# Performance work log

Measured on AMD Instinct MI355X. Metric: run time of the kernel, lower is better.

The kernel has to match this reference:

```python
import jax, jax.numpy as jnp
import numpy as np

N_NODES = 100000
N_EDGES = 3200000
N_FEAT = 512
HIDDEN = 16
N_CLASSES = 40


def gcn_conv(x, src, dst, W, b, num_nodes):
    # GCNConv with self-loops and symmetric normalization (default PyG settings).
    loop = jnp.arange(num_nodes)
    s = jnp.concatenate([src, loop])
    d = jnp.concatenate([dst, loop])
    deg = jax.ops.segment_sum(jnp.ones_like(s, dtype=x.dtype), d, num_segments=num_nodes)
    dinv = jnp.where(deg > 0, jax.lax.rsqrt(deg), 0.0)
    norm = dinv[s] * dinv[d]  # [E+N]
    h = x @ W  # [N, out]
    msg = h[s] * norm[:, None]  # gather + scale
    out = jax.ops.segment_sum(msg, d, num_segments=num_nodes)  # scatter-add
    return out + b


def setup_inputs() -> dict:
    key = jax.random.key(0)
    k1, k2, k3, k4 = jax.random.split(key, 4)
    x = jax.random.normal(k1, (N_NODES, N_FEAT), dtype=jnp.float32)
    edge_index = jax.random.randint(k2, (2, N_EDGES), 0, N_NODES, dtype=jnp.int64)
    W1 = jax.random.normal(k3, (N_FEAT, HIDDEN), dtype=jnp.float32) * 0.05
    b1 = jnp.zeros((HIDDEN,), dtype=jnp.float32)
    W2 = jax.random.normal(k4, (HIDDEN, N_CLASSES), dtype=jnp.float32) * 0.05
    b2 = jnp.zeros((N_CLASSES,), dtype=jnp.float32)
    return {"x": x, "edge_index": edge_index, "W1": W1, "b1": b1, "W2": W2, "b2": b2}


def reference(x, edge_index, W1, b1, W2, b2):
    num_nodes = x.shape[0]
    src, dst = edge_index[0], edge_index[1]
    h = gcn_conv(x, src, dst, W1, b1, num_nodes)
    h = jax.nn.relu(h)
    # dropout is identity in eval mode (training=False)
    out = gcn_conv(h, src, dst, W2, b2, num_nodes)
    return jax.nn.log_softmax(out, axis=1)
```

## Files before the change

kernel.cpp:

```cpp
#include <hip/hip_runtime.h>

#define N_NODES 100000
#define N_EDGES 3200000
#define N_FEAT 512
#define HIDDEN 16
#define N_CLASSES 40

#define SCAN_BLOCKS 98


__global__ void k_zero_int(int* p, int n) {
    int i = blockIdx.x * 256 + threadIdx.x;
    if (i < n) p[i] = 0;
}

__global__ void k_count(const int* __restrict__ dst, int* __restrict__ cnt,
                        int* __restrict__ ord) {
    int e = blockIdx.x * 256 + threadIdx.x;
    if (e < N_EDGES) ord[e] = atomicAdd(cnt + dst[e], 1);
}

__global__ void k_dinv(const int* __restrict__ cnt, float* __restrict__ dinv) {
    int i = blockIdx.x * 256 + threadIdx.x;
    if (i < N_NODES) dinv[i] = rsqrtf((float)(cnt[i] + 1));
}


__global__ __launch_bounds__(1024) void k_scan_a(const int* __restrict__ cnt,
                                                 int* __restrict__ bsum) {
    int tid = threadIdx.x;
    int i = blockIdx.x * 1024 + tid;
    int v = (i < N_NODES) ? cnt[i] : 0;
    #pragma unroll
    for (int off = 32; off >= 1; off >>= 1) v += __shfl_xor(v, off, 64);
    __shared__ int ws[16];
    if ((tid & 63) == 0) ws[tid >> 6] = v;
    __syncthreads();
    if (tid == 0) {
        int s = 0;
        #pragma unroll
        for (int w = 0; w < 16; w++) s += ws[w];
        bsum[blockIdx.x] = s;
    }
}

__global__ __launch_bounds__(128) void k_scan_b(const int* __restrict__ bsum,
                                                int* __restrict__ boff) {
    int tid = threadIdx.x;
    int lane = tid & 63, wv = tid >> 6;
    int v = (tid < SCAN_BLOCKS) ? bsum[tid] : 0;
    int sc = v;
    #pragma unroll
    for (int off = 1; off < 64; off <<= 1) {
        int t = __shfl_up(sc, off, 64);
        if (lane >= off) sc += t;
    }
    __shared__ int wsum[2];
    if (lane == 63) wsum[wv] = sc;
    __syncthreads();
    int pre = (wv == 1) ? wsum[0] : 0;
    if (tid < SCAN_BLOCKS) boff[tid] = pre + sc - v;
}

__global__ __launch_bounds__(1024) void k_scan_c(const int* __restrict__ cnt,
                                                 const int* __restrict__ boff,
                                                 int* __restrict__ row_start) {
    int tid = threadIdx.x;
    int i = blockIdx.x * 1024 + tid;
    int lane = tid & 63, wv = tid >> 6;
    int v = (i < N_NODES) ? cnt[i] : 0;
    int sc = v;
    #pragma unroll
    for (int off = 1; off < 64; off <<= 1) {
        int t = __shfl_up(sc, off, 64);
        if (lane >= off) sc += t;
    }
    __shared__ int wsum[16];
    if (lane == 63) wsum[wv] = sc;
    __syncthreads();
    int pre = 0;
    #pragma unroll
    for (int w = 0; w < 16; w++) pre += (w < wv) ? wsum[w] : 0;
    int excl = boff[blockIdx.x] + pre + sc - v;
    if (i < N_NODES) row_start[i] = excl;
    if (i == N_NODES) row_start[N_NODES] = N_EDGES;
}

__global__ void k_build(const int* __restrict__ src, const int* __restrict__ dst,
                        const int* __restrict__ ord, const int* __restrict__ row_start,
                        const float* __restrict__ dinv, int2* __restrict__ edge_data) {
    int e = blockIdx.x * 256 + threadIdx.x;
    if (e >= N_EDGES) return;
    int s = src[e], d = dst[e];
    int slot = row_start[d] + ord[e];
    float nrm = dinv[s] * dinv[d];
    edge_data[slot] = make_int2(s, __float_as_int(nrm));
}


#define KC 32
#define LDSW 36

__global__ __launch_bounds__(256) void k_gemm1(const float* __restrict__ x,
                                               const float* __restrict__ W1,
                                               float* __restrict__ h1) {
    __shared__ float xs[256 * LDSW];
    int tid = threadIdx.x;
    int row = blockIdx.x * 256 + tid;

    float acc[HIDDEN];
    #pragma unroll
    for (int j = 0; j < HIDDEN; j++) acc[j] = 0.f;

    int s_sub = tid >> 3;
    int s_k4  = tid & 7;

    for (int kc = 0; kc < N_FEAT; kc += KC) {
        __syncthreads();
        #pragma unroll
        for (int l = 0; l < 8; l++) {
            int srow = s_sub + l * 32;
            int grow = blockIdx.x * 256 + srow;
            int gr = grow < N_NODES ? grow : N_NODES - 1;
            float4 v = *reinterpret_cast<const float4*>(
                x + (size_t)gr * N_FEAT + kc + s_k4 * 4);
            *reinterpret_cast<float4*>(&xs[srow * LDSW + s_k4 * 4]) = v;
        }
        __syncthreads();

        const float* Wc = W1 + kc * HIDDEN;
        #pragma unroll
        for (int k4 = 0; k4 < 8; k4++) {
            float4 xv = *reinterpret_cast<const float4*>(&xs[tid * LDSW + k4 * 4]);
            const float* w0 = Wc + (k4 * 4 + 0) * HIDDEN;
            const float* w1 = Wc + (k4 * 4 + 1) * HIDDEN;
            const float* w2 = Wc + (k4 * 4 + 2) * HIDDEN;
            const float* w3 = Wc + (k4 * 4 + 3) * HIDDEN;
            #pragma unroll
            for (int j = 0; j < HIDDEN; j++) {
                acc[j] += xv.x * w0[j];
                acc[j] += xv.y * w1[j];
                acc[j] += xv.z * w2[j];
                acc[j] += xv.w * w3[j];
            }
        }
    }

    if (row < N_NODES) {
        float4* op = reinterpret_cast<float4*>(h1 + (size_t)row * HIDDEN);
        #pragma unroll
        for (int q = 0; q < 4; q++)
            op[q] = make_float4(acc[q*4+0], acc[q*4+1], acc[q*4+2], acc[q*4+3]);
    }
}


template <bool RELU>
__global__ __launch_bounds__(256) void k_agg16(const int2* __restrict__ edge_data,
                                               const int* __restrict__ row_start,
                                               const float* __restrict__ dinv,
                                               const float* __restrict__ h,
                                               const float* __restrict__ bias,
                                               float* __restrict__ out) {
    int g = threadIdx.x >> 4, j = threadIdx.x & 15;
    int node = blockIdx.x * 16 + g;
    if (node >= N_NODES) return;
    int beg = row_start[node], end = row_start[node + 1];
    float ds = dinv[node];
    float acc = h[(size_t)node * HIDDEN + j] * (ds * ds);
    int i = beg;
    for (; i + 3 < end; i += 4) {
        int2 e0 = edge_data[i + 0];
        int2 e1 = edge_data[i + 1];
        int2 e2 = edge_data[i + 2];
        int2 e3 = edge_data[i + 3];
        float v0 = h[(size_t)e0.x * HIDDEN + j];
        float v1 = h[(size_t)e1.x * HIDDEN + j];
        float v2 = h[(size_t)e2.x * HIDDEN + j];
        float v3 = h[(size_t)e3.x * HIDDEN + j];
        acc += v0 * __int_as_float(e0.y);
        acc += v1 * __int_as_float(e1.y);
        acc += v2 * __int_as_float(e2.y);
        acc += v3 * __int_as_float(e3.y);
    }
    for (; i < end; ++i) {
        int2 ed = edge_data[i];
        acc += h[(size_t)ed.x * HIDDEN + j] * __int_as_float(ed.y);
    }
    if (RELU) acc = fmaxf(acc + bias[j], 0.f);
    out[(size_t)node * HIDDEN + j] = acc;
}


__global__ __launch_bounds__(256) void k_out(const float* __restrict__ agg2,
                                             const float* __restrict__ W2,
                                             const float* __restrict__ b2,
                                             float* __restrict__ out) {
    int r = blockIdx.x * 256 + threadIdx.x;
    if (r >= N_NODES) return;
    float a[HIDDEN];
    const float4* ap = reinterpret_cast<const float4*>(agg2 + (size_t)r * HIDDEN);
    #pragma unroll
    for (int q = 0; q < 4; q++) {
        float4 v = ap[q];
        a[q * 4 + 0] = v.x; a[q * 4 + 1] = v.y;
        a[q * 4 + 2] = v.z; a[q * 4 + 3] = v.w;
    }
    float acc[N_CLASSES];
    #pragma unroll
    for (int jj = 0; jj < N_CLASSES; jj++) acc[jj] = b2[jj];
    #pragma unroll
    for (int kk = 0; kk < HIDDEN; kk++) {
        float av = a[kk];
        #pragma unroll
        for (int jj = 0; jj < N_CLASSES; jj++)
            acc[jj] += av * W2[kk * N_CLASSES + jj];
    }
    float m = -1e30f;
    #pragma unroll
    for (int jj = 0; jj < N_CLASSES; jj++) m = fmaxf(m, acc[jj]);
    float sum = 0.f;
    #pragma unroll
    for (int jj = 0; jj < N_CLASSES; jj++) sum += __expf(acc[jj] - m);
    float l = m + __logf(sum);
    float4* op = reinterpret_cast<float4*>(out + (size_t)r * N_CLASSES);
    #pragma unroll
    for (int q = 0; q < N_CLASSES / 4; q++) {
        op[q] = make_float4(acc[q*4+0] - l, acc[q*4+1] - l,
                            acc[q*4+2] - l, acc[q*4+3] - l);
    }
}


extern "C" void kernel_launch(void* const* d_in, const int* in_sizes, int n_in,
                              void* d_out, int out_size, void* d_ws, size_t ws_size,
                              hipStream_t stream) {
    const float* x  = (const float*)d_in[0];
    const int*   ei = (const int*)d_in[1];
    const float* W1 = (const float*)d_in[2];
    const float* b1 = (const float*)d_in[3];
    const float* W2 = (const float*)d_in[4];
    const float* b2 = (const float*)d_in[5];
    const int* src = ei;
    const int* dst = ei + N_EDGES;
    float* out = (float*)d_out;

    char* ws = (char*)d_ws;
    size_t off = 0;
    auto alloc = [&](size_t bytes) {
        size_t o = off; off = (off + bytes + 255) & ~(size_t)255; return o;
    };
    float* dinv      = (float*)(ws + alloc(sizeof(float) * N_NODES));
    int*   cnt       = (int*)  (ws + alloc(sizeof(int) * N_NODES));
    int*   row_start = (int*)  (ws + alloc(sizeof(int) * (N_NODES + 1)));
    int*   ord       = (int*)  (ws + alloc(sizeof(int) * N_EDGES));
    int2*  edge_data = (int2*) (ws + alloc(sizeof(int2) * N_EDGES));
    float* h1        = (float*)(ws + alloc(sizeof(float) * N_NODES * HIDDEN));
    float* rbuf      = (float*)(ws + alloc(sizeof(float) * N_NODES * HIDDEN));
    float* agg2      = (float*)(ws + alloc(sizeof(float) * N_NODES * HIDDEN));
    int*   bsum      = (int*)  (ws + alloc(sizeof(int) * SCAN_BLOCKS));
    int*   boff      = (int*)  (ws + alloc(sizeof(int) * SCAN_BLOCKS));

    const int nodeBlocks  = (N_NODES + 255) / 256;
    const int edgeBlocks  = (N_EDGES + 255) / 256;
    const int aggBlocks   = (N_NODES + 15) / 16;

    k_zero_int<<<nodeBlocks, 256, 0, stream>>>(cnt, N_NODES);
    k_count<<<edgeBlocks, 256, 0, stream>>>(dst, cnt, ord);
    k_dinv<<<nodeBlocks, 256, 0, stream>>>(cnt, dinv);
    k_scan_a<<<SCAN_BLOCKS, 1024, 0, stream>>>(cnt, bsum);
    k_scan_b<<<1, 128, 0, stream>>>(bsum, boff);
    k_scan_c<<<SCAN_BLOCKS, 1024, 0, stream>>>(cnt, boff, row_start);
    k_build<<<edgeBlocks, 256, 0, stream>>>(src, dst, ord, row_start, dinv, edge_data);

    k_gemm1<<<nodeBlocks, 256, 0, stream>>>(x, W1, h1);
    k_agg16<true><<<aggBlocks, 256, 0, stream>>>(edge_data, row_start, dinv, h1, b1, rbuf);
    k_agg16<false><<<aggBlocks, 256, 0, stream>>>(edge_data, row_start, dinv, rbuf, nullptr, agg2);
    k_out<<<nodeBlocks, 256, 0, stream>>>(agg2, W2, b2, out);
}
```

Baseline: 682.1 us.

## Build CSR via LDS-privatized per-range histograms instead of global atomics

Replaces global atomic counting of destinations with a two-pass scheme. Blocks partitioned by node range and edge slice count destinations in shared-memory histograms, a reduce kernel turns the per-slice counts into prefix offsets and totals, and the build pass re-derives each edge's slot with LDS atomics. This removes contended global atomics and the ord array, and the partial-histogram buffer reuses the hidden-feature workspace. In exchange every block rescans its whole dst slice once per node range (seven times overall), and edge ordering within a row is no longer deterministic.

```diff
diff --git a/kernel.cpp b/kernel.cpp
--- a/kernel.cpp
+++ b/kernel.cpp
@@ -8,16 +8,50 @@
 
 #define SCAN_BLOCKS 98
 
-
-__global__ void k_zero_int(int* p, int n) {
-    int i = blockIdx.x * 256 + threadIdx.x;
-    if (i < n) p[i] = 0;
-}
-
-__global__ void k_count(const int* __restrict__ dst, int* __restrict__ cnt,
-                        int* __restrict__ ord) {
-    int e = blockIdx.x * 256 + threadIdx.x;
-    if (e < N_EDGES) ord[e] = atomicAdd(cnt + dst[e], 1);
+#define NR 7
+#define RSH 14
+#define BINS 16384
+#define SL 32
+#define EPS 100000
+
+
+__global__ __launch_bounds__(256) void k_hist(const int* __restrict__ dst,
+                                              int* __restrict__ P) {
+    __shared__ int lds[BINS];
+    int r = blockIdx.x >> 5, s = blockIdx.x & 31;
+    int tid = threadIdx.x;
+    for (int t = tid; t < BINS; t += 256) lds[t] = 0;
+    __syncthreads();
+    int lo = r << RSH;
+    const int4* dp = reinterpret_cast<const int4*>(dst + s * EPS);
+    for (int i = tid; i < EPS / 4; i += 256) {
+        int4 d4 = dp[i];
+        int u;
+        u = d4.x - lo; if ((unsigned)u < BINS) atomicAdd(&lds[u], 1);
+        u = d4.y - lo; if ((unsigned)u < BINS) atomicAdd(&lds[u], 1);
+        u = d4.z - lo; if ((unsigned)u < BINS) atomicAdd(&lds[u], 1);
+        u = d4.w - lo; if ((unsigned)u < BINS) atomicAdd(&lds[u], 1);
+    }
+    __syncthreads();
+    int* Pb = P + (size_t)blockIdx.x * BINS;
+    for (int t = tid; t < BINS; t += 256) Pb[t] = lds[t];
+}
+
+
+__global__ __launch_bounds__(256) void k_reduce(int* __restrict__ P,
+                                                int* __restrict__ cnt) {
+    int n = blockIdx.x * 256 + threadIdx.x;
+    if (n >= N_NODES) return;
+    int r = n >> RSH, b = n & (BINS - 1);
+    int* p = P + (size_t)(r * SL) * BINS + b;
+    int sum = 0;
+    #pragma unroll
+    for (int s = 0; s < SL; s++) {
+        int v = p[(size_t)s * BINS];
+        p[(size_t)s * BINS] = sum;
+        sum += v;
+    }
+    cnt[n] = sum;
 }
 
 __global__ void k_dinv(const int* __restrict__ cnt, float* __restrict__ dinv) {
@@ -86,15 +120,38 @@
     if (i == N_NODES) row_start[N_NODES] = N_EDGES;
 }
 
-__global__ void k_build(const int* __restrict__ src, const int* __restrict__ dst,
-                        const int* __restrict__ ord, const int* __restrict__ row_start,
-                        const float* __restrict__ dinv, int2* __restrict__ edge_data) {
-    int e = blockIdx.x * 256 + threadIdx.x;
-    if (e >= N_EDGES) return;
-    int s = src[e], d = dst[e];
-    int slot = row_start[d] + ord[e];
-    float nrm = dinv[s] * dinv[d];
-    edge_data[slot] = make_int2(s, __float_as_int(nrm));
+
+__global__ __launch_bounds__(256) void k_build2(const int* __restrict__ src,
+                                                const int* __restrict__ dst,
+                                                const int* __restrict__ P,
+                                                const int* __restrict__ row_start,
+                                                const float* __restrict__ dinv,
+                                                int2* __restrict__ edge_data) {
+    __shared__ int lds[BINS];
+    int r = blockIdx.x >> 5, s = blockIdx.x & 31;
+    int tid = threadIdx.x;
+    const int* Pb = P + (size_t)blockIdx.x * BINS;
+    for (int t = tid; t < BINS; t += 256) lds[t] = Pb[t];
+    __syncthreads();
+    int lo = r << RSH;
+    int base = s * EPS;
+    const int4* dp = reinterpret_cast<const int4*>(dst + base);
+    for (int i = tid; i < EPS / 4; i += 256) {
+        int4 d4 = dp[i];
+        int e = base + i * 4;
+        int dd[4] = {d4.x, d4.y, d4.z, d4.w};
+        #pragma unroll
+        for (int q = 0; q < 4; q++) {
+            int d = dd[q];
+            int u = d - lo;
+            if ((unsigned)u < BINS) {
+                int ord = atomicAdd(&lds[u], 1);
+                int sv = src[e + q];
+                float nrm = dinv[sv] * dinv[d];
+                edge_data[row_start[d] + ord] = make_int2(sv, __float_as_int(nrm));
+            }
+        }
+    }
 }
 
 
@@ -253,25 +310,28 @@
     float* dinv      = (float*)(ws + alloc(sizeof(float) * N_NODES));
     int*   cnt       = (int*)  (ws + alloc(sizeof(int) * N_NODES));
     int*   row_start = (int*)  (ws + alloc(sizeof(int) * (N_NODES + 1)));
-    int*   ord       = (int*)  (ws + alloc(sizeof(int) * N_EDGES));
-    int2*  edge_data = (int2*) (ws + alloc(sizeof(int2) * N_EDGES));
-    float* h1        = (float*)(ws + alloc(sizeof(float) * N_NODES * HIDDEN));
-    float* rbuf      = (float*)(ws + alloc(sizeof(float) * N_NODES * HIDDEN));
-    float* agg2      = (float*)(ws + alloc(sizeof(float) * N_NODES * HIDDEN));
     int*   bsum      = (int*)  (ws + alloc(sizeof(int) * SCAN_BLOCKS));
     int*   boff      = (int*)  (ws + alloc(sizeof(int) * SCAN_BLOCKS));
-
-    const int nodeBlocks  = (N_NODES + 255) / 256;
-    const int edgeBlocks  = (N_EDGES + 255) / 256;
-    const int aggBlocks   = (N_NODES + 15) / 16;
-
-    k_zero_int<<<nodeBlocks, 256, 0, stream>>>(cnt, N_NODES);
-    k_count<<<edgeBlocks, 256, 0, stream>>>(dst, cnt, ord);
+    int2*  edge_data = (int2*) (ws + alloc(sizeof(int2) * N_EDGES));
+    size_t pBytes = sizeof(int) * (size_t)NR * SL * BINS;
+    size_t hBytes = sizeof(float) * (size_t)N_NODES * HIDDEN * 3;
+    char*  big = ws + alloc(pBytes > hBytes ? pBytes : hBytes);
+    int*   P    = (int*)big;
+    float* h1   = (float*)big;
+    float* rbuf = h1 + (size_t)N_NODES * HIDDEN;
+    float* agg2 = rbuf + (size_t)N_NODES * HIDDEN;
+
+    const int nodeBlocks = (N_NODES + 255) / 256;
+    const int histBlocks = NR * SL;
+    const int aggBlocks  = (N_NODES + 15) / 16;
+
+    k_hist<<<histBlocks, 256, 0, stream>>>(dst, P);
+    k_reduce<<<nodeBlocks, 256, 0, stream>>>(P, cnt);
     k_dinv<<<nodeBlocks, 256, 0, stream>>>(cnt, dinv);
     k_scan_a<<<SCAN_BLOCKS, 1024, 0, stream>>>(cnt, bsum);
     k_scan_b<<<1, 128, 0, stream>>>(bsum, boff);
     k_scan_c<<<SCAN_BLOCKS, 1024, 0, stream>>>(cnt, boff, row_start);
-    k_build<<<edgeBlocks, 256, 0, stream>>>(src, dst, ord, row_start, dinv, edge_data);
+    k_build2<<<histBlocks, 256, 0, stream>>>(src, dst, P, row_start, dinv, edge_data);
 
     k_gemm1<<<nodeBlocks, 256, 0, stream>>>(x, W1, h1);
     k_agg16<true><<<aggBlocks, 256, 0, stream>>>(edge_data, row_start, dinv, h1, b1, rbuf);
```

New measurement: 719.0 us. +5.4%, slower.
